# Kernel optimization log

Measured on AMD Instinct MI355X. Metric: run time of the kernel, lower is better.

The kernel has to match this reference:

```python
import jax, jax.numpy as jnp
import numpy as np

N, E, G = 64, 128, 4
D0, ED = 9, 4
H1, H2, H3 = 2000, 500, 100
F1, F2, F3 = 1000, 100, 50


def setup_inputs() -> dict:
    key = jax.random.key(0)
    ks = iter(jax.random.split(key, 32))

    def p(shape, s=0.02):
        return (jax.random.normal(next(ks), shape, jnp.float32) * s)

    inp = {
        "x": jax.random.normal(next(ks), (N, D0), jnp.float32),
        "edge_index": jax.random.randint(next(ks), (2, E), 0, N),
        "edge_attr": jax.random.normal(next(ks), (E, ED), jnp.float32),
        "batch": jnp.sort(jax.random.randint(next(ks), (N,), 0, G)),
        # NNConv layer 1: edge MLP Linear(ED, D0*H1), root weight, bias
        "We1": p((ED, D0 * H1)), "be1": p((D0 * H1,)),
        "root1": p((D0, H1)), "b1": p((H1,)),
        # NNConv layer 2
        "We2": p((ED, H1 * H2)), "be2": p((H1 * H2,)),
        "root2": p((H1, H2)), "b2": p((H2,)),
        # NNConv layer 3
        "We3": p((ED, H2 * H3)), "be3": p((H2 * H3,)),
        "root3": p((H2, H3)), "b3": p((H3,)),
        # FCN head
        "W1": p((H3, F1)), "c1": p((F1,)),
        "W2": p((F1, F2)), "c2": p((F2,)),
        "W3": p((F2, F3)), "c3": p((F3,)),
        "W4": p((F3, 1)), "c4": p((1,)),
    }
    return inp


def _nnconv(x, src, dst, edge_attr, We, be, root, b):
    # edge-conditioned weights: [E, in, out]
    in_dim = x.shape[1]
    w = (edge_attr @ We + be).reshape(edge_attr.shape[0], in_dim, -1)
    # gather source feats, per-edge matmul, scatter-add to targets
    msg = jnp.einsum('ei,eio->eo', x[src], w)
    agg = jax.ops.segment_sum(msg, dst, num_segments=x.shape[0])
    return agg + x @ root + b


def reference(x, edge_index, edge_attr, batch,
              We1, be1, root1, b1,
              We2, be2, root2, b2,
              We3, be3, root3, b3,
              W1, c1, W2, c2, W3, c3, W4, c4):
    src, dst = edge_index[0], edge_index[1]
    h = jax.nn.relu(_nnconv(x, src, dst, edge_attr, We1, be1, root1, b1))
    h = jax.nn.relu(_nnconv(h, src, dst, edge_attr, We2, be2, root2, b2))
    h = jax.nn.relu(_nnconv(h, src, dst, edge_attr, We3, be3, root3, b3))
    # sum readout per graph (dropout layers are identity in eval mode)
    g = jax.ops.segment_sum(h, batch, num_segments=G)  # [G, H3]
    g = jax.nn.relu(g @ W1 + c1)
    g = jax.nn.relu(g @ W2 + c2)
    g = jax.nn.relu(g @ W3 + c3)
    out = g @ W4 + c4
    return out.reshape(-1)  # [G]
```

## Files before the change

kernel.cpp:

```cpp
#include <hip/hip_runtime.h>

#define NN 64
#define EE 128
#define GG 4
#define D0 9
#define H1 2000
#define H2 500
#define H3 100
#define FF1 1000
#define FF2 100
#define FF3 50

#define OFF_P1   28032
#define OFF_Q    156032
#define OFF_PART 924032
#define OFF_P2   4124032
#define OFF_PRE3 4156032
#define OFF_F1   4162432
#define OFF_PH   4166448

__device__ __forceinline__ void gl2lds16(const float* g, float* l) {
    __builtin_amdgcn_global_load_lds(
        (const __attribute__((address_space(1))) unsigned int*)g,
        (__attribute__((address_space(3))) unsigned int*)l,
        16, 0, 0);
}

__device__ __forceinline__ float4 ldf4(const float* p) {
    return *(const float4*)p;
}

__device__ __forceinline__ void waitcnt_vm_n(int n) {
    switch (n) {
    case 0: asm volatile("s_waitcnt vmcnt(0)" ::: "memory"); break;
    case 2: asm volatile("s_waitcnt vmcnt(2)" ::: "memory"); break;
    case 4: asm volatile("s_waitcnt vmcnt(4)" ::: "memory"); break;
    default: asm volatile("s_waitcnt vmcnt(6)" ::: "memory"); break;
    }
}
__device__ __forceinline__ void cfence() { asm volatile("" ::: "memory"); }

template<int NR>
__device__ __forceinline__ void build_Ad_rows(float* Al, int d, int v0,
    const int* __restrict__ ei, const float* __restrict__ ea, int tid)
{
    for (int i = tid; i < NR * 64; i += 256) Al[i] = 0.f;
    __syncthreads();
    if (d == 5) {
        if (tid >= v0 && tid < v0 + NR && tid < NN)
            Al[(tid - v0) * 64 + tid] = 1.0f;
    } else if (tid < EE) {
        int s = ei[tid], t = ei[EE + tid];
        if (t >= v0 && t < v0 + NR) {
            float v = (d < 4) ? ea[tid * 4 + d] : 1.0f;
            atomicAdd(&Al[(t - v0) * 64 + s], v);
        }
    }
}

template<int Kd, int KTOT, int NRG>
__device__ __forceinline__ void q_compute_store(
    const float* Al, const float* Pl, float* __restrict__ Qf,
    int d, int k0, int v0, int tid)
{
    const int kq = tid & 31, rg = tid >> 5;
    float acc[NRG][4] = {};
    #pragma unroll 4
    for (int u4 = 0; u4 < 16; ++u4) {
        float4 pv0 = ldf4(&Pl[(u4 * 4 + 0) * 128 + kq * 4]);
        float4 pv1 = ldf4(&Pl[(u4 * 4 + 1) * 128 + kq * 4]);
        float4 pv2 = ldf4(&Pl[(u4 * 4 + 2) * 128 + kq * 4]);
        float4 pv3 = ldf4(&Pl[(u4 * 4 + 3) * 128 + kq * 4]);
        #pragma unroll
        for (int i = 0; i < NRG; ++i) {
            float4 a = ldf4(&Al[(rg * NRG + i) * 64 + u4 * 4]);
            acc[i][0] += a.x * pv0.x + a.y * pv1.x + a.z * pv2.x + a.w * pv3.x;
            acc[i][1] += a.x * pv0.y + a.y * pv1.y + a.z * pv2.y + a.w * pv3.y;
            acc[i][2] += a.x * pv0.z + a.y * pv1.z + a.z * pv2.z + a.w * pv3.z;
            acc[i][3] += a.x * pv0.w + a.y * pv1.w + a.z * pv2.w + a.w * pv3.w;
        }
    }
    const int k = k0 + kq * 4;
    if (k < Kd) {
        #pragma unroll
        for (int i = 0; i < NRG; ++i) {
            int r = v0 + rg * NRG + i;
            *(float4*)(Qf + r * KTOT + d * Kd + k) =
                make_float4(acc[i][0], acc[i][1], acc[i][2], acc[i][3]);
        }
    }
}

__global__ __launch_bounds__(256) void k_p1(
    const float* __restrict__ x, const int* __restrict__ edge_index,
    const float* __restrict__ edge_attr,
    const float* __restrict__ We1, const float* __restrict__ be1,
    const float* __restrict__ root1, const float* __restrict__ b1,
    float* __restrict__ P1)
{
    __shared__ float Ys[64 * 56];
    __shared__ __align__(16) float Bs[54 * 64];
    const int tid = threadIdx.x;
    const int tx = tid & 15, ty = tid >> 4;
    const int o0 = blockIdx.x * 64;
    const int w = min(64, H1 - o0);

    for (int i = tid; i < 64 * 56; i += 256) Ys[i] = 0.f;
    __syncthreads();
    if (tid < EE) {
        int s = edge_index[tid], t = edge_index[EE + tid];
        float ea[4];
        #pragma unroll
        for (int d = 0; d < 4; ++d) ea[d] = edge_attr[tid * 4 + d];
        #pragma unroll
        for (int i = 0; i < D0; ++i) {
            float xv = x[s * D0 + i];
            #pragma unroll
            for (int d = 0; d < 4; ++d)
                atomicAdd(&Ys[t * 56 + d * 9 + i], ea[d] * xv);
            atomicAdd(&Ys[t * 56 + 36 + i], xv);
        }
    }
    if (tid < NN) {
        #pragma unroll
        for (int i = 0; i < D0; ++i) Ys[tid * 56 + 45 + i] = x[tid * D0 + i];
    }
    for (int i = tid; i < 54 * 64; i += 256) {
        int r = i >> 6, c = i & 63;
        int d = r / 9, ii = r - d * 9;
        const float* rowp = ((d < 4) ? (We1 + d * (D0 * H1))
                                     : ((d == 4) ? be1 : root1)) + ii * H1;
        Bs[r * 64 + c] = (c < w) ? rowp[o0 + c] : 0.f;
    }
    __syncthreads();

    float acc[4][4] = {};
    #pragma unroll 6
    for (int r = 0; r < 54; ++r) {
        float a0 = Ys[(ty * 4 + 0) * 56 + r];
        float a1 = Ys[(ty * 4 + 1) * 56 + r];
        float a2 = Ys[(ty * 4 + 2) * 56 + r];
        float a3 = Ys[(ty * 4 + 3) * 56 + r];
        const float4 bv = *(const float4*)&Bs[r * 64 + tx * 4];
        acc[0][0] += a0 * bv.x; acc[0][1] += a0 * bv.y; acc[0][2] += a0 * bv.z; acc[0][3] += a0 * bv.w;
        acc[1][0] += a1 * bv.x; acc[1][1] += a1 * bv.y; acc[1][2] += a1 * bv.z; acc[1][3] += a1 * bv.w;
        acc[2][0] += a2 * bv.x; acc[2][1] += a2 * bv.y; acc[2][2] += a2 * bv.z; acc[2][3] += a2 * bv.w;
        acc[3][0] += a3 * bv.x; acc[3][1] += a3 * bv.y; acc[3][2] += a3 * bv.z; acc[3][3] += a3 * bv.w;
    }
    #pragma unroll
    for (int i = 0; i < 4; ++i) {
        int u = ty * 4 + i;
        #pragma unroll
        for (int jj = 0; jj < 4; ++jj) {
            int j = o0 + tx * 4 + jj;
            if (j < H1) {
                float v = b1[j] + acc[i][jj];
                P1[u * H1 + j] = v > 0.f ? v : 0.f;
            }
        }
    }
}

template<int Kd, int KTOT, int NKT, int RS>
__global__ __launch_bounds__(256) void k_qp(
    const int* __restrict__ edge_index, const float* __restrict__ edge_attr,
    const float* __restrict__ P, float* __restrict__ Qf)
{
    constexpr int NR = 64 / RS;
    __shared__ __align__(16) float Al[NR * 64];
    __shared__ __align__(16) float Pl[64 * 128];
    const int tid = threadIdx.x;
    const int bx = blockIdx.x;
    const int d = bx / (NKT * RS);
    const int rem = bx % (NKT * RS);
    const int kt = rem / RS, rh = rem % RS;
    const int k0 = kt * 128;
    const int v0 = rh * NR;
    const int nf4 = (min(128, Kd - k0) + 3) >> 2;

    build_Ad_rows<NR>(Al, d, v0, edge_index, edge_attr, tid);
    for (int i4 = tid; i4 < 2048; i4 += 256) {
        int u = i4 >> 5, c4 = i4 & 31;
        float4 v = {0.f, 0.f, 0.f, 0.f};
        if (c4 < nf4) v = ldf4(P + u * Kd + k0 + c4 * 4);
        *(float4*)&Pl[u * 128 + c4 * 4] = v;
    }
    __syncthreads();
    q_compute_store<Kd, KTOT, NR / 8>(Al, Pl, Qf, d, k0, v0, tid);
}

template<int M, int S, int ITERS, int T1, int T2>
__global__ __launch_bounds__(256) void k_split(
    const float* __restrict__ Qf, const float* __restrict__ We,
    const float* __restrict__ be, const float* __restrict__ root,
    float* __restrict__ part)
{
    constexpr int KC = 20, BN = 64;
    constexpr int KTOT = S * ITERS * KC;
    const int b = blockIdx.x;
    const int s = b % S, ot = b / S;
    const int o0 = ot * BN;
    const int tid = threadIdx.x;
    const int tx = tid & 15, ty = tid >> 4;
    const int wv = tid >> 6, ln = tid & 63;
    const int kbase = s * (KC * ITERS);
    const int nw = (wv == 0) ? 4 : 2;

    __shared__ __align__(16) float As[2][64 * KC];
    __shared__ __align__(16) float Bs[2][KC * BN];

    auto stage = [&](int bf, int kb) {
        for (int c = wv; c < 5; c += 4) {
            int f = c * 256 + ln * 4;
            int r = f / KC, kkk = f - r * KC;
            gl2lds16(Qf + r * KTOT + kb + kkk, &As[bf][c * 256]);
        }
        for (int c = wv; c < 5; c += 4) {
            int f = c * 256 + ln * 4;
            int krow = f >> 6, col = f & 63;
            int kg = kb + krow;
            const float* bp = (kg < T1) ? (We + (long long)kg * M)
                            : (kg < T2) ? (be + (long long)(kg - T1) * M)
                                        : (root + (long long)(kg - T2) * M);
            int cc = min(o0 + col, M - 4);
            gl2lds16(bp + cc, &Bs[bf][c * 256]);
        }
    };

    float acc[4][4] = {};
    stage(0, kbase);
    for (int it = 0; it < ITERS; ++it) {
        int npend = 0;
        if (it + 1 < ITERS) { stage((it + 1) & 1, kbase + (it + 1) * KC); npend = nw; }
        waitcnt_vm_n(npend);
        __builtin_amdgcn_s_barrier();
        __builtin_amdgcn_sched_barrier(0);

        const float* Ab = As[it & 1];
        const float* Bb = Bs[it & 1];
        #pragma unroll
        for (int k4 = 0; k4 < 5; ++k4) {
            float4 av[4], bv[4];
            #pragma unroll
            for (int i = 0; i < 4; ++i)
                av[i] = ldf4(&Ab[(ty * 4 + i) * KC + k4 * 4]);
            #pragma unroll
            for (int q = 0; q < 4; ++q)
                bv[q] = ldf4(&Bb[(k4 * 4 + q) * BN + tx * 4]);
            #pragma unroll
            for (int i = 0; i < 4; ++i) {
                acc[i][0] += av[i].x * bv[0].x; acc[i][1] += av[i].x * bv[0].y;
                acc[i][2] += av[i].x * bv[0].z; acc[i][3] += av[i].x * bv[0].w;
                acc[i][0] += av[i].y * bv[1].x; acc[i][1] += av[i].y * bv[1].y;
                acc[i][2] += av[i].y * bv[1].z; acc[i][3] += av[i].y * bv[1].w;
                acc[i][0] += av[i].z * bv[2].x; acc[i][1] += av[i].z * bv[2].y;
                acc[i][2] += av[i].z * bv[2].z; acc[i][3] += av[i].z * bv[2].w;
                acc[i][0] += av[i].w * bv[3].x; acc[i][1] += av[i].w * bv[3].y;
                acc[i][2] += av[i].w * bv[3].z; acc[i][3] += av[i].w * bv[3].w;
            }
        }
        cfence();
        __builtin_amdgcn_sched_barrier(0);
        __builtin_amdgcn_s_barrier();
    }

    float* dst = part + s * (64 * M);
    #pragma unroll
    for (int i = 0; i < 4; ++i) {
        int u = ty * 4 + i;
        #pragma unroll
        for (int jj = 0; jj < 4; ++jj) {
            int j = o0 + tx * 4 + jj;
            if (j < M) dst[u * M + j] = acc[i][jj];
        }
    }
}

template<int NS>
__global__ __launch_bounds__(256) void k_red2(
    const float* __restrict__ part, const float* __restrict__ b2,
    float* __restrict__ P2)
{
    int i4 = blockIdx.x * 256 + threadIdx.x;
    if (i4 >= (64 * 500) / 4) return;
    int o = (i4 * 4) % 500;
    float4 acc = ldf4(b2 + o);
    #pragma unroll 10
    for (int s = 0; s < NS; ++s) {
        float4 v = ldf4(part + s * 32000 + i4 * 4);
        acc.x += v.x; acc.y += v.y; acc.z += v.z; acc.w += v.w;
    }
    acc.x = fmaxf(acc.x, 0.f); acc.y = fmaxf(acc.y, 0.f);
    acc.z = fmaxf(acc.z, 0.f); acc.w = fmaxf(acc.w, 0.f);
    *(float4*)(P2 + i4 * 4) = acc;
}

template<int NS>
__global__ __launch_bounds__(256) void k_red3(
    const float* __restrict__ part, const float* __restrict__ b3,
    float* __restrict__ pre3)
{
    int i4 = blockIdx.x * 256 + threadIdx.x;
    if (i4 >= (64 * 100) / 4) return;
    int o = (i4 * 4) % 100;
    float4 acc = ldf4(b3 + o);
    #pragma unroll 10
    for (int s = 0; s < NS; ++s) {
        float4 v = ldf4(part + s * 6400 + i4 * 4);
        acc.x += v.x; acc.y += v.y; acc.z += v.z; acc.w += v.w;
    }
    *(float4*)(pre3 + i4 * 4) = acc;
}

__global__ __launch_bounds__(256) void k_head1(
    const float* __restrict__ pre3, const int* __restrict__ batch,
    const float* __restrict__ W1, const float* __restrict__ c1,
    float* __restrict__ f1)
{
    const int gi = blockIdx.x >> 4;
    const int jt = blockIdx.x & 15;
    const int o0 = jt * 64;
    const int tid = threadIdx.x;
    __shared__ int   bsh[NN];
    __shared__ float gs[H3];
    __shared__ float red[4 * 64];

    if (tid < NN) bsh[tid] = batch[tid];
    __syncthreads();
    for (int d = tid; d < H3; d += 256) {
        float acc = 0.f;
        #pragma unroll
        for (int v = 0; v < NN; ++v) {
            float h = pre3[v * H3 + d];
            h = h > 0.f ? h : 0.f;
            acc += (bsh[v] == gi) ? h : 0.f;
        }
        gs[d] = acc;
    }
    __syncthreads();
    const int jj = tid & 63, kq = tid >> 6;
    const int oc = min(o0 + jj, FF1 - 1);
    float p = 0.f;
    #pragma unroll
    for (int k = kq * 25; k < kq * 25 + 25; ++k)
        p += gs[k] * W1[k * FF1 + oc];
    red[kq * 64 + jj] = p;
    __syncthreads();
    if (tid < 64) {
        int o = o0 + tid;
        if (o < FF1) {
            float v = c1[o] + red[tid] + red[64 + tid] + red[128 + tid] + red[192 + tid];
            f1[gi * FF1 + o] = v > 0.f ? v : 0.f;
        }
    }
}

__global__ __launch_bounds__(256) void k_h2(
    const float* __restrict__ f1, const float* __restrict__ W2,
    float* __restrict__ ph)
{
    const int s = blockIdx.x;
    const int k0 = s * 40;
    const int tid = threadIdx.x;
    __shared__ float f1s[GG * 40];
    for (int i = tid; i < GG * 40; i += 256) {
        int gi = i / 40, kk = i - gi * 40;
        f1s[i] = f1[gi * FF1 + k0 + kk];
    }
    __syncthreads();
    for (int idx = tid; idx < GG * FF2; idx += 256) {
        int gi = idx / FF2, o = idx - gi * FF2;
        float acc = 0.f;
        #pragma unroll 8
        for (int kk = 0; kk < 40; ++kk)
            acc += f1s[gi * 40 + kk] * W2[(k0 + kk) * FF2 + o];
        ph[s * (GG * FF2) + idx] = acc;
    }
}

__global__ __launch_bounds__(256) void k_head3(
    const float* __restrict__ ph, const float* __restrict__ c2,
    const float* __restrict__ W3, const float* __restrict__ c3,
    const float* __restrict__ W4, const float* __restrict__ c4,
    float* __restrict__ out)
{
    const int tid = threadIdx.x;
    __shared__ float f2s[GG * FF2];
    __shared__ float f3s[GG * FF3];
    for (int idx = tid; idx < GG * FF2; idx += 256) {
        int o = idx % FF2;
        float acc = c2[o];
        #pragma unroll 5
        for (int s = 0; s < 25; ++s) acc += ph[s * (GG * FF2) + idx];
        f2s[idx] = acc > 0.f ? acc : 0.f;
    }
    __syncthreads();
    if (tid < GG * FF3) {
        int gi = tid / FF3, o = tid - gi * FF3;
        float acc = c3[o];
        #pragma unroll 4
        for (int k = 0; k < FF2; ++k)
            acc += f2s[gi * FF2 + k] * W3[k * FF3 + o];
        f3s[tid] = acc > 0.f ? acc : 0.f;
    }
    __syncthreads();
    if (tid < GG) {
        float acc = c4[0];
        #pragma unroll
        for (int k = 0; k < FF3; ++k) acc += f3s[tid * FF3 + k] * W4[k];
        out[tid] = acc;
    }
}

extern "C" void kernel_launch(void* const* d_in, const int* in_sizes, int n_in,
                              void* d_out, int out_size, void* d_ws, size_t ws_size,
                              hipStream_t stream) {
    const float* x          = (const float*)d_in[0];
    const int*   edge_index = (const int*)  d_in[1];
    const float* edge_attr  = (const float*)d_in[2];
    const int*   batch      = (const int*)  d_in[3];
    const float* We1 = (const float*)d_in[4];
    const float* be1 = (const float*)d_in[5];
    const float* root1 = (const float*)d_in[6];
    const float* b1  = (const float*)d_in[7];
    const float* We2 = (const float*)d_in[8];
    const float* be2 = (const float*)d_in[9];
    const float* root2 = (const float*)d_in[10];
    const float* b2  = (const float*)d_in[11];
    const float* We3 = (const float*)d_in[12];
    const float* be3 = (const float*)d_in[13];
    const float* root3 = (const float*)d_in[14];
    const float* b3  = (const float*)d_in[15];
    const float* W1 = (const float*)d_in[16];
    const float* c1 = (const float*)d_in[17];
    const float* W2 = (const float*)d_in[18];
    const float* c2 = (const float*)d_in[19];
    const float* W3 = (const float*)d_in[20];
    const float* c3 = (const float*)d_in[21];
    const float* W4 = (const float*)d_in[22];
    const float* c4 = (const float*)d_in[23];
    float* ws  = (float*)d_ws;
    float* out = (float*)d_out;

    k_p1<<<32, 256, 0, stream>>>(x, edge_index, edge_attr,
                                 We1, be1, root1, b1, ws + OFF_P1);
    k_qp<2000, 12000, 16, 2><<<192, 256, 0, stream>>>(edge_index, edge_attr,
                                                      ws + OFF_P1, ws + OFF_Q);
    k_split<500, 100, 6, 8000, 10000><<<800, 256, 0, stream>>>(
        ws + OFF_Q, We2, be2, root2, ws + OFF_PART);
    k_red2<100><<<32, 256, 0, stream>>>(ws + OFF_PART, b2, ws + OFF_P2);
    k_qp<500, 3000, 4, 2><<<48, 256, 0, stream>>>(edge_index, edge_attr,
                                                  ws + OFF_P2, ws + OFF_Q);
    k_split<100, 150, 1, 2000, 2500><<<300, 256, 0, stream>>>(
        ws + OFF_Q, We3, be3, root3, ws + OFF_PART);
    k_red3<150><<<7, 256, 0, stream>>>(ws + OFF_PART, b3, ws + OFF_PRE3);
    k_head1<<<64, 256, 0, stream>>>(ws + OFF_PRE3, batch, W1, c1,
                                    ws + OFF_F1);
    k_h2<<<25, 256, 0, stream>>>(ws + OFF_F1, W2, ws + OFF_PH);
    k_head3<<<1, 256, 0, stream>>>(ws + OFF_PH, c2, W3, c3, W4, c4, out);
}
```

Baseline: 204.4 us.

## Fuse layer-1 transform into Q computation and merge head tail via last-block counter

Removes two kernel launches. The first layer's per-node transform (P1) is now computed inside the kernel that builds the per-edge Q tiles, so P1 no longer takes a round-trip through global memory. Each of the 96 blocks recomputes its 128-column P1 slice for its own d index, which duplicates that work six times. The final head stages are folded into the W2 partial kernel: an atomic counter, reset in k_red3, lets the last block finish the reduction and the W3/W4 layers.

New measurement: 208.7 us. 1.02x slower.

```diff
diff --git a/kernel.cpp b/kernel.cpp
--- a/kernel.cpp
+++ b/kernel.cpp
@@ -11,13 +11,13 @@
 #define FF2 100
 #define FF3 50
 
-#define OFF_P1   28032
 #define OFF_Q    156032
 #define OFF_PART 924032
 #define OFF_P2   4124032
 #define OFF_PRE3 4156032
 #define OFF_F1   4162432
 #define OFF_PH   4166448
+#define OFF_CNT  4176448
 
 __device__ __forceinline__ void gl2lds16(const float* g, float* l) {
     __builtin_amdgcn_global_load_lds(
@@ -91,19 +91,20 @@
     }
 }
 
-__global__ __launch_bounds__(256) void k_p1(
+__global__ __launch_bounds__(256) void k_pq2(
     const float* __restrict__ x, const int* __restrict__ edge_index,
     const float* __restrict__ edge_attr,
     const float* __restrict__ We1, const float* __restrict__ be1,
     const float* __restrict__ root1, const float* __restrict__ b1,
-    float* __restrict__ P1)
-{
-    __shared__ float Ys[64 * 56];
-    __shared__ __align__(16) float Bs[54 * 64];
+    float* __restrict__ Qf)
+{
+    __shared__ __align__(16) float sm[12288];
+    float* Ys = sm;
+    float* Bs = sm + 3584;
     const int tid = threadIdx.x;
-    const int tx = tid & 15, ty = tid >> 4;
-    const int o0 = blockIdx.x * 64;
-    const int w = min(64, H1 - o0);
+    const int d = blockIdx.x >> 4, kt = blockIdx.x & 15;
+    const int k0 = kt * 128;
+    const int kq = tid & 31, rg = tid >> 5;
 
     for (int i = tid; i < 64 * 56; i += 256) Ys[i] = 0.f;
     __syncthreads();
@@ -111,13 +112,13 @@
         int s = edge_index[tid], t = edge_index[EE + tid];
         float ea[4];
         #pragma unroll
-        for (int d = 0; d < 4; ++d) ea[d] = edge_attr[tid * 4 + d];
+        for (int dd = 0; dd < 4; ++dd) ea[dd] = edge_attr[tid * 4 + dd];
         #pragma unroll
         for (int i = 0; i < D0; ++i) {
             float xv = x[s * D0 + i];
             #pragma unroll
-            for (int d = 0; d < 4; ++d)
-                atomicAdd(&Ys[t * 56 + d * 9 + i], ea[d] * xv);
+            for (int dd = 0; dd < 4; ++dd)
+                atomicAdd(&Ys[t * 56 + dd * 9 + i], ea[dd] * xv);
             atomicAdd(&Ys[t * 56 + 36 + i], xv);
         }
     }
@@ -125,40 +126,54 @@
         #pragma unroll
         for (int i = 0; i < D0; ++i) Ys[tid * 56 + 45 + i] = x[tid * D0 + i];
     }
-    for (int i = tid; i < 54 * 64; i += 256) {
-        int r = i >> 6, c = i & 63;
-        int d = r / 9, ii = r - d * 9;
-        const float* rowp = ((d < 4) ? (We1 + d * (D0 * H1))
-                                     : ((d == 4) ? be1 : root1)) + ii * H1;
-        Bs[r * 64 + c] = (c < w) ? rowp[o0 + c] : 0.f;
-    }
-    __syncthreads();
-
-    float acc[4][4] = {};
-    #pragma unroll 6
+    for (int i = tid; i < 54 * 128; i += 256) {
+        int r = i >> 7, c = i & 127;
+        int dd = r / 9, ii = r - dd * 9;
+        const float* rowp = ((dd < 4) ? (We1 + dd * (D0 * H1))
+                                      : ((dd == 4) ? be1 : root1)) + ii * H1;
+        Bs[i] = (k0 + c < H1) ? rowp[k0 + c] : 0.f;
+    }
+    __syncthreads();
+
+    const int j0 = k0 + kq * 4;
+    float b1v[4];
+    #pragma unroll
+    for (int jj = 0; jj < 4; ++jj)
+        b1v[jj] = (j0 + jj < H1) ? b1[j0 + jj] : 0.f;
+    float p[8][4] = {};
     for (int r = 0; r < 54; ++r) {
-        float a0 = Ys[(ty * 4 + 0) * 56 + r];
-        float a1 = Ys[(ty * 4 + 1) * 56 + r];
-        float a2 = Ys[(ty * 4 + 2) * 56 + r];
-        float a3 = Ys[(ty * 4 + 3) * 56 + r];
-        const float4 bv = *(const float4*)&Bs[r * 64 + tx * 4];
-        acc[0][0] += a0 * bv.x; acc[0][1] += a0 * bv.y; acc[0][2] += a0 * bv.z; acc[0][3] += a0 * bv.w;
-        acc[1][0] += a1 * bv.x; acc[1][1] += a1 * bv.y; acc[1][2] += a1 * bv.z; acc[1][3] += a1 * bv.w;
-        acc[2][0] += a2 * bv.x; acc[2][1] += a2 * bv.y; acc[2][2] += a2 * bv.z; acc[2][3] += a2 * bv.w;
-        acc[3][0] += a3 * bv.x; acc[3][1] += a3 * bv.y; acc[3][2] += a3 * bv.z; acc[3][3] += a3 * bv.w;
-    }
+        const float4 bv = ldf4(&Bs[r * 128 + kq * 4]);
+        #pragma unroll
+        for (int i = 0; i < 8; ++i) {
+            float a = Ys[(rg * 8 + i) * 56 + r];
+            p[i][0] += a * bv.x; p[i][1] += a * bv.y;
+            p[i][2] += a * bv.z; p[i][3] += a * bv.w;
+        }
+    }
+    __syncthreads();
+
+    float* Pl = sm;
+    float* Al = sm + 8192;
     #pragma unroll
-    for (int i = 0; i < 4; ++i) {
-        int u = ty * 4 + i;
-        #pragma unroll
-        for (int jj = 0; jj < 4; ++jj) {
-            int j = o0 + tx * 4 + jj;
-            if (j < H1) {
-                float v = b1[j] + acc[i][jj];
-                P1[u * H1 + j] = v > 0.f ? v : 0.f;
-            }
-        }
-    }
+    for (int i = 0; i < 8; ++i) {
+        float4 v;
+        v.x = fmaxf(b1v[0] + p[i][0], 0.f);
+        v.y = fmaxf(b1v[1] + p[i][1], 0.f);
+        v.z = fmaxf(b1v[2] + p[i][2], 0.f);
+        v.w = fmaxf(b1v[3] + p[i][3], 0.f);
+        *(float4*)&Pl[(rg * 8 + i) * 128 + kq * 4] = v;
+    }
+    for (int i = tid; i < 4096; i += 256) Al[i] = 0.f;
+    __syncthreads();
+    if (d == 5) {
+        if (tid < NN) Al[tid * 64 + tid] = 1.0f;
+    } else if (tid < EE) {
+        int s = edge_index[tid], t = edge_index[EE + tid];
+        float v = (d < 4) ? edge_attr[tid * 4 + d] : 1.0f;
+        atomicAdd(&Al[t * 64 + s], v);
+    }
+    __syncthreads();
+    q_compute_store<2000, 12000, 8>(Al, Pl, Qf, d, k0, 0, tid);
 }
 
 template<int Kd, int KTOT, int NKT, int RS>
@@ -298,8 +313,9 @@
 template<int NS>
 __global__ __launch_bounds__(256) void k_red3(
     const float* __restrict__ part, const float* __restrict__ b3,
-    float* __restrict__ pre3)
-{
+    float* __restrict__ pre3, int* __restrict__ cnt)
+{
+    if (blockIdx.x == 0 && threadIdx.x == 0) *cnt = 0;
     int i4 = blockIdx.x * 256 + threadIdx.x;
     if (i4 >= (64 * 100) / 4) return;
     int o = (i4 * 4) % 100;
@@ -355,14 +371,21 @@
     }
 }
 
-__global__ __launch_bounds__(256) void k_h2(
+__global__ __launch_bounds__(256) void k_h23(
     const float* __restrict__ f1, const float* __restrict__ W2,
-    float* __restrict__ ph)
+    const float* __restrict__ c2, const float* __restrict__ W3,
+    const float* __restrict__ c3, const float* __restrict__ W4,
+    const float* __restrict__ c4, float* __restrict__ ph,
+    int* __restrict__ cnt, float* __restrict__ out)
 {
     const int s = blockIdx.x;
     const int k0 = s * 40;
     const int tid = threadIdx.x;
     __shared__ float f1s[GG * 40];
+    __shared__ float f2s[GG * FF2];
+    __shared__ float f3s[GG * FF3];
+    __shared__ int lastFlag;
+
     for (int i = tid; i < GG * 40; i += 256) {
         int gi = i / 40, kk = i - gi * 40;
         f1s[i] = f1[gi * FF1 + k0 + kk];
@@ -376,22 +399,20 @@
             acc += f1s[gi * 40 + kk] * W2[(k0 + kk) * FF2 + o];
         ph[s * (GG * FF2) + idx] = acc;
     }
-}
-
-__global__ __launch_bounds__(256) void k_head3(
-    const float* __restrict__ ph, const float* __restrict__ c2,
-    const float* __restrict__ W3, const float* __restrict__ c3,
-    const float* __restrict__ W4, const float* __restrict__ c4,
-    float* __restrict__ out)
-{
-    const int tid = threadIdx.x;
-    __shared__ float f2s[GG * FF2];
-    __shared__ float f3s[GG * FF3];
+    __syncthreads();
+    if (tid == 0) {
+        int prev = __hip_atomic_fetch_add(cnt, 1, __ATOMIC_ACQ_REL,
+                                          __HIP_MEMORY_SCOPE_AGENT);
+        lastFlag = (prev == 24);
+    }
+    __syncthreads();
+    if (!lastFlag) return;
+
     for (int idx = tid; idx < GG * FF2; idx += 256) {
         int o = idx % FF2;
         float acc = c2[o];
         #pragma unroll 5
-        for (int s = 0; s < 25; ++s) acc += ph[s * (GG * FF2) + idx];
+        for (int sl = 0; sl < 25; ++sl) acc += ph[sl * (GG * FF2) + idx];
         f2s[idx] = acc > 0.f ? acc : 0.f;
     }
     __syncthreads();
@@ -442,10 +463,8 @@
     float* ws  = (float*)d_ws;
     float* out = (float*)d_out;
 
-    k_p1<<<32, 256, 0, stream>>>(x, edge_index, edge_attr,
-                                 We1, be1, root1, b1, ws + OFF_P1);
-    k_qp<2000, 12000, 16, 2><<<192, 256, 0, stream>>>(edge_index, edge_attr,
-                                                      ws + OFF_P1, ws + OFF_Q);
+    k_pq2<<<96, 256, 0, stream>>>(x, edge_index, edge_attr,
+                                  We1, be1, root1, b1, ws + OFF_Q);
     k_split<500, 100, 6, 8000, 10000><<<800, 256, 0, stream>>>(
         ws + OFF_Q, We2, be2, root2, ws + OFF_PART);
     k_red2<100><<<32, 256, 0, stream>>>(ws + OFF_PART, b2, ws + OFF_P2);
@@ -453,9 +472,10 @@
                                                   ws + OFF_P2, ws + OFF_Q);
     k_split<100, 150, 1, 2000, 2500><<<300, 256, 0, stream>>>(
         ws + OFF_Q, We3, be3, root3, ws + OFF_PART);
-    k_red3<150><<<7, 256, 0, stream>>>(ws + OFF_PART, b3, ws + OFF_PRE3);
+    k_red3<150><<<7, 256, 0, stream>>>(ws + OFF_PART, b3, ws + OFF_PRE3,
+                                       (int*)(ws + OFF_CNT));
     k_head1<<<64, 256, 0, stream>>>(ws + OFF_PRE3, batch, W1, c1,
                                     ws + OFF_F1);
-    k_h2<<<25, 256, 0, stream>>>(ws + OFF_F1, W2, ws + OFF_PH);
-    k_head3<<<1, 256, 0, stream>>>(ws + OFF_PH, c2, W3, c3, W4, c4, out);
-}
+    k_h23<<<25, 256, 0, stream>>>(ws + OFF_F1, W2, c2, W3, c3, W4, c4,
+                                  ws + OFF_PH, (int*)(ws + OFF_CNT), out);
+}
```
